# Kernel optimization log

Measured on AMD Instinct MI355X. Metric: run time of the kernel, lower is better.

The kernel has to match this reference:

```python
import jax, jax.numpy as jnp
import numpy as np

B, S, H = 8, 2048, 1024

def setup_inputs() -> dict:
    key = jax.random.key(0)
    k1, k2, k3 = jax.random.split(key, 3)
    lstm_out = jax.random.normal(k1, (B, S, H), dtype=jnp.float32)
    # nn.Linear(hidden_size, hidden_size): weight [H, H], bias [H]
    W = jax.random.normal(k2, (H, H), dtype=jnp.float32) * (1.0 / np.sqrt(H))
    b = jax.random.normal(k3, (H,), dtype=jnp.float32) * 0.01
    return {"lstm_out": lstm_out, "W": W, "b": b}

def reference(lstm_out, W, b):
    # out = linear(lstm_out)  (torch Linear: x @ W.T + b)
    out = jnp.einsum('bsh,oh->bso', lstm_out, W) + b            # [B,S,H]
    # score = bmm(out, out^T)  -- unscaled, Q = K
    score = jnp.einsum('bqh,bkh->bqk', out, out)                # [B,S,S]
    attn = jax.nn.softmax(score, axis=-1)                       # [B,S,S]
    # context = bmm(attn, lstm_out)
    context = jnp.einsum('bqk,bkh->bqh', attn, lstm_out)        # [B,S,H]
    return context
```

## Files before the change

### kernel.cpp

```cpp
#include <hip/hip_runtime.h>
#include <hip/hip_bf16.h>
#include <stdint.h>

#define BB 8
#define SS 2048
#define HH 1024

typedef __bf16 bf16_t;
typedef bf16_t bf16x8 __attribute__((ext_vector_type(8)));
typedef float f32x4 __attribute__((ext_vector_type(4)));
typedef unsigned short u16x8 __attribute__((ext_vector_type(8)));

__device__ __forceinline__ unsigned short f2bf(float f) {
    unsigned int u = __float_as_uint(f);
    u += 0x7fffu + ((u >> 16) & 1u);
    return (unsigned short)(u >> 16);
}
__device__ __forceinline__ float bf2f(unsigned short h) {
    return __uint_as_float((unsigned int)h << 16);
}

__global__ __launch_bounds__(256) void cast_f32_bf16(
    const float* __restrict__ in, unsigned short* __restrict__ out, int n4)
{
    int i = blockIdx.x * blockDim.x + threadIdx.x;
    int stride = gridDim.x * blockDim.x;
    for (; i < n4; i += stride) {
        float4 v = reinterpret_cast<const float4*>(in)[i];
        ushort4 o;
        o.x = f2bf(v.x); o.y = f2bf(v.y); o.z = f2bf(v.z); o.w = f2bf(v.w);
        reinterpret_cast<ushort4*>(out)[i] = o;
    }
}

__global__ __launch_bounds__(256) void transpose_cast(
    const float* __restrict__ in,
    unsigned short* __restrict__ outN,
    unsigned short* __restrict__ outT)
{
    __shared__ float tile[32][33];
    const int tx = threadIdx.x, ty = threadIdx.y;
    const int h0 = blockIdx.x * 32, s0 = blockIdx.y * 32, b = blockIdx.z;
    const float* src = in + ((size_t)b * SS + s0) * HH + h0;
    unsigned short* dN = outN + ((size_t)b * SS + s0) * HH + h0;
    unsigned short* dT = outT + ((size_t)b * HH + h0) * SS + s0;
#pragma unroll
    for (int i = 0; i < 4; i++) {
        float v = src[(size_t)(ty + i * 8) * HH + tx];
        tile[ty + i * 8][tx] = v;
        dN[(size_t)(ty + i * 8) * HH + tx] = f2bf(v);
    }
    __syncthreads();
#pragma unroll
    for (int i = 0; i < 4; i++) {
        dT[(size_t)(ty + i * 8) * SS + tx] = f2bf(tile[tx][ty + i * 8]);
    }
}

__global__ __launch_bounds__(256) void softmax_rows_bf16(unsigned short* __restrict__ score)
{
    const size_t row = blockIdx.x;
    unsigned short* srow = score + row * 2048;
    const int t = threadIdx.x;
    const int wave = t >> 6, lane = t & 63;

    u16x8 v = *reinterpret_cast<u16x8*>(srow + (size_t)t * 8);
    float x[8];
#pragma unroll
    for (int i = 0; i < 8; i++) x[i] = bf2f(v[i]);

    float m = x[0];
#pragma unroll
    for (int i = 1; i < 8; i++) m = fmaxf(m, x[i]);
#pragma unroll
    for (int off = 32; off; off >>= 1) m = fmaxf(m, __shfl_xor(m, off));

    __shared__ float red[4];
    if (!lane) red[wave] = m;
    __syncthreads();
    m = fmaxf(fmaxf(red[0], red[1]), fmaxf(red[2], red[3]));

    float e[8];
    float s = 0.0f;
#pragma unroll
    for (int i = 0; i < 8; i++) { e[i] = __expf(x[i] - m); s += e[i]; }
#pragma unroll
    for (int off = 32; off; off >>= 1) s += __shfl_xor(s, off);
    __syncthreads();
    if (!lane) red[wave] = s;
    __syncthreads();
    s = red[0] + red[1] + red[2] + red[3];
    const float inv = 1.0f / s;

    u16x8 o;
#pragma unroll
    for (int i = 0; i < 8; i++) o[i] = f2bf(e[i] * inv);
    *reinterpret_cast<u16x8*>(srow + (size_t)t * 8) = o;
}

#define GLL16(gp, lp)                                                        \
    __builtin_amdgcn_global_load_lds(                                        \
        (const __attribute__((address_space(1))) unsigned int*)(gp),         \
        (__attribute__((address_space(3))) unsigned int*)(lp), 16, 0, 0)

template <int OUT_BF16, int HAS_BIAS>
__global__ __launch_bounds__(512, 2) void gemm_nt_256(
    const unsigned short* __restrict__ A, long long aBatch, int lda,
    const unsigned short* __restrict__ Bm, long long bBatch, int ldb,
    void* __restrict__ Cp, long long cBatch, int ldc,
    const float* __restrict__ bias, int K, int GXT)
{
    __shared__ unsigned short lds[3 * 16384];

    const int tid = threadIdx.x;
    const int wave = tid >> 6, lane = tid & 63;
    const int wr = wave >> 2, wc = wave & 3;
    const int fr = lane & 15, fc = lane >> 4;

    const int q = gridDim.x >> 3;
    const int x = blockIdx.x;
    const int wgid = (x & 7) * q + (x >> 3);
    const int bx = wgid % GXT, by = wgid / GXT;

    const unsigned short* Ap = A + (size_t)blockIdx.z * aBatch + (size_t)by * 256 * lda;
    const unsigned short* Bp = Bm + (size_t)blockIdx.z * bBatch + (size_t)bx * 256 * ldb;

    const int sr = tid >> 2;
    const int sc = tid & 3;
    const int r0 = sr, r1 = sr + 128;
    const unsigned short* sA0 = Ap + (size_t)r0 * lda + ((sc ^ ((r0 >> 1) & 3)) << 3);
    const unsigned short* sA1 = Ap + (size_t)r1 * lda + ((sc ^ ((r1 >> 1) & 3)) << 3);
    const unsigned short* sB0 = Bp + (size_t)r0 * ldb + ((sc ^ ((r0 >> 1) & 3)) << 3);
    const unsigned short* sB1 = Bp + (size_t)r1 * ldb + ((sc ^ ((r1 >> 1) & 3)) << 3);
    const int dA0 = wave * 512;
    const int dA1 = 4096 + wave * 512;

    const int kch = ((fc ^ ((fr >> 1) & 3)) << 3);
    int offA[8], offB[4];
#pragma unroll
    for (int m = 0; m < 8; m++) offA[m] = (wr * 128 + m * 16 + fr) * 32 + kch;
#pragma unroll
    for (int n = 0; n < 4; n++) offB[n] = (wc * 64 + n * 16 + fr) * 32 + kch;

    f32x4 acc[8][4];
    const f32x4 zero = {0.0f, 0.0f, 0.0f, 0.0f};
#pragma unroll
    for (int m = 0; m < 8; m++)
#pragma unroll
        for (int n = 0; n < 4; n++) acc[m][n] = zero;

    const int NT = K >> 5;

    {
        unsigned short* b0 = lds;
        unsigned short* b1 = lds + 16384;
        GLL16(sA0, b0 + dA0); GLL16(sA1, b0 + dA1);
        GLL16(sB0, b0 + 8192 + dA0); GLL16(sB1, b0 + 8192 + dA1);
        GLL16(sA0 + 32, b1 + dA0); GLL16(sA1 + 32, b1 + dA1);
        GLL16(sB0 + 32, b1 + 8192 + dA0); GLL16(sB1 + 32, b1 + 8192 + dA1);
    }
    asm volatile("s_waitcnt vmcnt(4)" ::: "memory");
    __builtin_amdgcn_sched_barrier(0);
    __builtin_amdgcn_s_barrier();

    for (int t = 0; t < NT; ++t) {
        const int cur = t % 3;
        const int nb = (t + 2) % 3;
        const int sk = (t + 2 < NT ? t + 2 : NT - 1) << 5;
        const unsigned short* tA = lds + cur * 16384;
        const unsigned short* tB = tA + 8192;
        unsigned short* nA = lds + nb * 16384;
        unsigned short* nB = nA + 8192;

        bf16x8 a0[4], b0[4];
#pragma unroll
        for (int m = 0; m < 4; m++)
            a0[m] = *reinterpret_cast<const bf16x8*>(tA + offA[m]);
#pragma unroll
        for (int n = 0; n < 4; n++)
            b0[n] = *reinterpret_cast<const bf16x8*>(tB + offB[n]);
        GLL16(sA0 + sk, nA + dA0);
        GLL16(sA1 + sk, nA + dA1);
        __builtin_amdgcn_s_barrier();
        __builtin_amdgcn_s_setprio(1);
#pragma unroll
        for (int m = 0; m < 4; m++)
#pragma unroll
            for (int n = 0; n < 4; n++)
                acc[m][n] = __builtin_amdgcn_mfma_f32_16x16x32_bf16(a0[m], b0[n], acc[m][n], 0, 0, 0);
        __builtin_amdgcn_s_setprio(0);
        __builtin_amdgcn_s_barrier();

        bf16x8 a1[4];
#pragma unroll
        for (int m = 0; m < 4; m++)
            a1[m] = *reinterpret_cast<const bf16x8*>(tA + offA[4 + m]);
        GLL16(sB0 + sk, nB + dA0);
        GLL16(sB1 + sk, nB + dA1);
        __builtin_amdgcn_s_barrier();
        __builtin_amdgcn_s_setprio(1);
#pragma unroll
        for (int m = 0; m < 4; m++)
#pragma unroll
            for (int n = 0; n < 4; n++)
                acc[4 + m][n] = __builtin_amdgcn_mfma_f32_16x16x32_bf16(a1[m], b0[n], acc[4 + m][n], 0, 0, 0);
        __builtin_amdgcn_s_setprio(0);
        asm volatile("s_waitcnt vmcnt(4)" ::: "memory");
        __builtin_amdgcn_sched_barrier(0);
        __builtin_amdgcn_s_barrier();
    }
    asm volatile("s_waitcnt vmcnt(0)" ::: "memory");
    __builtin_amdgcn_sched_barrier(0);

    const int rBase = by * 256 + wr * 128 + fc * 4;
    const int cBase = bx * 256 + wc * 64 + fr;
    if (OUT_BF16) {
        unsigned short* C = (unsigned short*)Cp + (size_t)blockIdx.z * cBatch;
#pragma unroll
        for (int n = 0; n < 4; n++) {
            const int col = cBase + n * 16;
            const float bv = HAS_BIAS ? bias[col] : 0.0f;
#pragma unroll
            for (int m = 0; m < 8; m++) {
                const int row = rBase + m * 16;
#pragma unroll
                for (int j = 0; j < 4; j++)
                    C[(size_t)(row + j) * ldc + col] = f2bf(acc[m][n][j] + bv);
            }
        }
    } else {
        float* C = (float*)Cp + (size_t)blockIdx.z * cBatch;
#pragma unroll
        for (int n = 0; n < 4; n++) {
            const int col = cBase + n * 16;
#pragma unroll
            for (int m = 0; m < 8; m++) {
                const int row = rBase + m * 16;
#pragma unroll
                for (int j = 0; j < 4; j++)
                    C[(size_t)(row + j) * ldc + col] = acc[m][n][j];
            }
        }
    }
}

extern "C" void kernel_launch(void* const* d_in, const int* in_sizes, int n_in,
                              void* d_out, int out_size, void* d_ws, size_t ws_size,
                              hipStream_t stream)
{
    const float* lstm = (const float*)d_in[0];
    const float* W    = (const float*)d_in[1];
    const float* bias = (const float*)d_in[2];
    float* out = (float*)d_out;

    unsigned short* lstm_bf = (unsigned short*)d_ws;
    unsigned short* out_bf  = lstm_bf + (size_t)BB * SS * HH;
    unsigned short* lstmT   = out_bf + (size_t)BB * SS * HH;
    unsigned short* W_bf    = lstmT + (size_t)BB * HH * SS;
    unsigned short* score   = W_bf + (size_t)HH * HH;

    transpose_cast<<<dim3(HH / 32, SS / 32, BB), dim3(32, 8), 0, stream>>>(
        lstm, lstm_bf, lstmT);

    cast_f32_bf16<<<dim3(512), dim3(256), 0, stream>>>(W, W_bf, HH * HH / 4);

    gemm_nt_256<1, 1><<<dim3(256, 1, 1), dim3(512), 0, stream>>>(
        lstm_bf, 0, HH, W_bf, 0, HH, out_bf, 0, HH, bias, HH, HH / 256);

    gemm_nt_256<1, 0><<<dim3(64, 1, BB), dim3(512), 0, stream>>>(
        out_bf, (long long)SS * HH, HH,
        out_bf, (long long)SS * HH, HH,
        score, (long long)SS * SS, SS, nullptr, HH, SS / 256);

    softmax_rows_bf16<<<dim3(BB * SS), dim3(256), 0, stream>>>(score);

    gemm_nt_256<0, 0><<<dim3(32, 1, BB), dim3(512), 0, stream>>>(
        score, (long long)SS * SS, SS,
        lstmT, (long long)HH * SS, SS,
        out, (long long)SS * HH, HH, nullptr, SS, HH / 256);
}
```

Measured before the change: 349.5 us.

## Deepen GEMM LDS pipeline to four stages and vectorize transpose-cast

The GEMM kernel grows from a triple-buffered to a quad-buffered LDS ring, prefetching three K-tiles ahead and waiting with vmcnt(8), so more global-load latency is hidden. The cost is LDS use rising from 96KB to 128KB per block, which may not fit two blocks per CU under launch_bounds(512,2) and so may cut occupancy. Separately, the transpose-cast kernel now uses float4 loads and ushort4 stores for both the normal and transposed bf16 outputs. That gives wider global accesses, at the risk of more LDS bank conflicts on the strided transposed reads.

```diff
diff --git a/kernel.cpp b/kernel.cpp
--- a/kernel.cpp
+++ b/kernel.cpp
@@ -39,22 +39,27 @@
     unsigned short* __restrict__ outT)
 {
     __shared__ float tile[32][33];
-    const int tx = threadIdx.x, ty = threadIdx.y;
+    const int t = threadIdx.x;
+    const int row = t >> 3;
+    const int c4  = t & 7;
     const int h0 = blockIdx.x * 32, s0 = blockIdx.y * 32, b = blockIdx.z;
-    const float* src = in + ((size_t)b * SS + s0) * HH + h0;
-    unsigned short* dN = outN + ((size_t)b * SS + s0) * HH + h0;
-    unsigned short* dT = outT + ((size_t)b * HH + h0) * SS + s0;
-#pragma unroll
-    for (int i = 0; i < 4; i++) {
-        float v = src[(size_t)(ty + i * 8) * HH + tx];
-        tile[ty + i * 8][tx] = v;
-        dN[(size_t)(ty + i * 8) * HH + tx] = f2bf(v);
-    }
-    __syncthreads();
-#pragma unroll
-    for (int i = 0; i < 4; i++) {
-        dT[(size_t)(ty + i * 8) * SS + tx] = f2bf(tile[tx][ty + i * 8]);
-    }
+
+    const float* src = in + ((size_t)b * SS + s0 + row) * HH + h0 + c4 * 4;
+    const float4 v = *reinterpret_cast<const float4*>(src);
+    ushort4 o;
+    o.x = f2bf(v.x); o.y = f2bf(v.y); o.z = f2bf(v.z); o.w = f2bf(v.w);
+    *reinterpret_cast<ushort4*>(outN + ((size_t)b * SS + s0 + row) * HH + h0 + c4 * 4) = o;
+    tile[row][c4 * 4 + 0] = v.x;
+    tile[row][c4 * 4 + 1] = v.y;
+    tile[row][c4 * 4 + 2] = v.z;
+    tile[row][c4 * 4 + 3] = v.w;
+    __syncthreads();
+    ushort4 p;
+    p.x = f2bf(tile[c4 * 4 + 0][row]);
+    p.y = f2bf(tile[c4 * 4 + 1][row]);
+    p.z = f2bf(tile[c4 * 4 + 2][row]);
+    p.w = f2bf(tile[c4 * 4 + 3][row]);
+    *reinterpret_cast<ushort4*>(outT + ((size_t)b * HH + h0 + row) * SS + s0 + c4 * 4) = p;
 }
 
 __global__ __launch_bounds__(256) void softmax_rows_bf16(unsigned short* __restrict__ score)
@@ -110,7 +115,7 @@
     void* __restrict__ Cp, long long cBatch, int ldc,
     const float* __restrict__ bias, int K, int GXT)
 {
-    __shared__ unsigned short lds[3 * 16384];
+    __shared__ unsigned short lds[4 * 16384];
 
     const int tid = threadIdx.x;
     const int wave = tid >> 6, lane = tid & 63;
@@ -154,19 +159,22 @@
     {
         unsigned short* b0 = lds;
         unsigned short* b1 = lds + 16384;
+        unsigned short* b2 = lds + 32768;
         GLL16(sA0, b0 + dA0); GLL16(sA1, b0 + dA1);
         GLL16(sB0, b0 + 8192 + dA0); GLL16(sB1, b0 + 8192 + dA1);
         GLL16(sA0 + 32, b1 + dA0); GLL16(sA1 + 32, b1 + dA1);
         GLL16(sB0 + 32, b1 + 8192 + dA0); GLL16(sB1 + 32, b1 + 8192 + dA1);
-    }
-    asm volatile("s_waitcnt vmcnt(4)" ::: "memory");
+        GLL16(sA0 + 64, b2 + dA0); GLL16(sA1 + 64, b2 + dA1);
+        GLL16(sB0 + 64, b2 + 8192 + dA0); GLL16(sB1 + 64, b2 + 8192 + dA1);
+    }
+    asm volatile("s_waitcnt vmcnt(8)" ::: "memory");
     __builtin_amdgcn_sched_barrier(0);
     __builtin_amdgcn_s_barrier();
 
     for (int t = 0; t < NT; ++t) {
-        const int cur = t % 3;
-        const int nb = (t + 2) % 3;
-        const int sk = (t + 2 < NT ? t + 2 : NT - 1) << 5;
+        const int cur = t & 3;
+        const int nb = (t + 3) & 3;
+        const int sk = (t + 3 < NT ? t + 3 : NT - 1) << 5;
         const unsigned short* tA = lds + cur * 16384;
         const unsigned short* tB = tA + 8192;
         unsigned short* nA = lds + nb * 16384;
@@ -205,7 +213,7 @@
             for (int n = 0; n < 4; n++)
                 acc[4 + m][n] = __builtin_amdgcn_mfma_f32_16x16x32_bf16(a1[m], b0[n], acc[4 + m][n], 0, 0, 0);
         __builtin_amdgcn_s_setprio(0);
-        asm volatile("s_waitcnt vmcnt(4)" ::: "memory");
+        asm volatile("s_waitcnt vmcnt(8)" ::: "memory");
         __builtin_amdgcn_sched_barrier(0);
         __builtin_amdgcn_s_barrier();
     }
@@ -259,7 +267,7 @@
     unsigned short* W_bf    = lstmT + (size_t)BB * HH * SS;
     unsigned short* score   = W_bf + (size_t)HH * HH;
 
-    transpose_cast<<<dim3(HH / 32, SS / 32, BB), dim3(32, 8), 0, stream>>>(
+    transpose_cast<<<dim3(HH / 32, SS / 32, BB), dim3(256), 0, stream>>>(
         lstm, lstm_bf, lstmT);
 
     cast_f32_bf16<<<dim3(512), dim3(256), 0, stream>>>(W, W_bf, HH * HH / 4);
```

Measured after the change: 346.9 us. Within noise of the previous version (-0.7%).
